# Performance work log

Measured on AMD Instinct MI355X. Metric: run time of the kernel, lower is better.

The kernel has to match this reference:

```python
import jax, jax.numpy as jnp
import numpy as np

SR = 44100.0
BS, NT, SEQ = 2, 16, 262144
REV_N, TAPS = 65536, 1023

EQ_R = [(-12., 12.), (20., 2000.), (0.1, 5.0),
        (-12., 12.), (80., 2000.), (0.1, 5.0),
        (-12., 12.), (2000., 8000.), (0.1, 5.0),
        (-12., 12.), (8000., 12000.), (0.1, 5.0),
        (-12., 12.), (12000., 21050.), (0.1, 5.0),
        (-12., 12.), (6000., 21050.), (0.1, 5.0)]
COMP_R = [(-60., 0.), (1., 10.), (5., 250.), (10., 250.), (3., 12.), (0., 6.)]
TRACK_R = np.array([(-48., 48.)] + EQ_R + COMP_R + [(-80., 12.), (0., 1.)], np.float32)
MASTER_R = np.array([(-48., 48.)] + EQ_R + COMP_R + [(-48., 48.)], np.float32)


def _pow2(n):
    return 1 << int(np.ceil(np.log2(n)))


def _denorm(p, r):
    lo = jnp.asarray(r[:, 0])
    hi = jnp.asarray(r[:, 1])
    return p * (hi - lo) + lo


def _biquad(g_db, fc, q, ftype):
    # RBJ cookbook biquads, coefficients normalized by a0
    A = 10.0 ** (g_db / 40.0)
    w0 = 2.0 * np.pi * (fc / SR)
    al = jnp.sin(w0) / (2.0 * q)
    c = jnp.cos(w0)
    sA = jnp.sqrt(A)
    if ftype == 'low_shelf':
        b0 = A * ((A + 1) - (A - 1) * c + 2 * sA * al)
        b1 = 2 * A * ((A - 1) - (A + 1) * c)
        b2 = A * ((A + 1) - (A - 1) * c - 2 * sA * al)
        a0 = (A + 1) + (A - 1) * c + 2 * sA * al
        a1 = -2 * ((A - 1) + (A + 1) * c)
        a2 = (A + 1) + (A - 1) * c - 2 * sA * al
    elif ftype == 'high_shelf':
        b0 = A * ((A + 1) + (A - 1) * c + 2 * sA * al)
        b1 = -2 * A * ((A - 1) + (A + 1) * c)
        b2 = A * ((A + 1) + (A - 1) * c - 2 * sA * al)
        a0 = (A + 1) - (A - 1) * c + 2 * sA * al
        a1 = 2 * ((A - 1) - (A + 1) * c)
        a2 = (A + 1) - (A - 1) * c - 2 * sA * al
    else:  # peaking
        b0 = 1 + al * A
        b1 = -2 * c
        b2 = 1 - al * A
        a0 = 1 + al / A
        a1 = -2 * c
        a2 = 1 - al / A
    b = jnp.stack([b0, b1, b2], -1) / a0[..., None]
    a = jnp.stack([a0, a1, a2], -1) / a0[..., None]
    return b, a


def _apply_eq(x, p):
    # 6-section cascaded biquad EQ applied via frequency sampling (as dasp_pytorch does).
    # x: (..., S); p: (..., 18) broadcastable with x's leading dims.
    S = x.shape[-1]
    nfft = _pow2(2 * S - 1)
    nf = nfft // 2 + 1
    w = jnp.arange(nf, dtype=jnp.float32) * (2.0 * np.pi / nfft)
    z1 = jnp.exp(-1j * w)
    z2 = z1 * z1
    H = jnp.ones((nf,), jnp.complex64)
    for k, ftype in enumerate(['low_shelf', 'peaking', 'peaking', 'peaking', 'peaking', 'high_shelf']):
        b, a = _biquad(p[..., 3 * k], p[..., 3 * k + 1], p[..., 3 * k + 2], ftype)
        num = b[..., 0:1] + b[..., 1:2] * z1 + b[..., 2:3] * z2
        den = a[..., 0:1] + a[..., 1:2] * z1 + a[..., 2:3] * z2
        H = H * (num / den)
    X = jnp.fft.rfft(x, nfft)
    return jnp.fft.irfft(X * H, nfft)[..., :S].astype(x.dtype)


def _apply_comp(x, p, lookahead):
    # soft-knee compressor; gain smoothed by one-pole (attack) via frequency sampling.
    S = x.shape[-1]
    nfft = _pow2(2 * S - 1)
    nf = nfft // 2 + 1
    th, ratio, at_ms, rel_ms, knee, makeup = [p[..., i:i + 1] for i in range(6)]
    x_db = 20.0 * jnp.log10(jnp.maximum(jnp.abs(x), 1e-8))
    d = x_db - th
    x_sc = jnp.where(2.0 * d < -knee, x_db,
                     jnp.where(2.0 * jnp.abs(d) <= knee,
                               x_db + (1.0 / ratio - 1.0) * (d + knee / 2.0) ** 2 / (2.0 * knee),
                               th + d / ratio))
    g_c = x_sc - x_db  # gain reduction in dB (<= 0)
    alpha = jnp.exp(-jnp.log(9.0) / (SR * at_ms * 1e-3))  # (..., 1)
    w = jnp.arange(nf, dtype=jnp.float32) * (2.0 * np.pi / nfft)
    H = (1.0 - alpha) / (1.0 - alpha * jnp.exp(-1j * w))
    g_s = jnp.fft.irfft(jnp.fft.rfft(g_c, nfft) * H, nfft)[..., :S]
    if lookahead > 0:
        tail = jnp.repeat(g_s[..., -1:], lookahead, axis=-1)
        g_s = jnp.concatenate([g_s[..., lookahead:], tail], axis=-1)
    return (x * 10.0 ** ((g_s + makeup) / 20.0)).astype(x.dtype)


def _reverb(x, noise, fb, gains, decays, mix):
    # noise-shaped reverberation: 12 octave-band filtered noise bursts with
    # exponential decays summed into an IR, FFT-convolved with x, wet/dry mix.
    S = x.shape[-1]
    nL = _pow2(REV_N + TAPS - 1)
    filt = jnp.fft.irfft(jnp.fft.rfft(noise, nL) * jnp.fft.rfft(fb, nL), nL)
    filt = filt[..., TAPS - 1:TAPS - 1 + REV_N]  # (bs, 2, 12, REV_N) 'valid' part
    t = jnp.linspace(0.0, 1.0, REV_N)
    dec = decays * 10.0 + 1.0  # (bs, 12)
    env = jnp.exp(-dec[:, None, :, None] * t)
    ir = (filt * env * gains[:, None, :, None]).mean(axis=2)  # (bs, 2, REV_N)
    n2 = _pow2(S + REV_N - 1)
    wet = jnp.fft.irfft(jnp.fft.rfft(x, n2) * jnp.fft.rfft(ir, n2), n2)[..., :S]
    m = mix[:, None, None]
    return (1.0 - m) * x + m * wet


def _firwin_lp(numtaps, fc, fs):
    n = np.arange(numtaps) - (numtaps - 1) / 2.0
    h = (2.0 * fc / fs) * np.sinc(2.0 * fc / fs * n)
    h = h * np.hamming(numtaps)
    return h / h.sum()


def _octave_fb():
    centers = [31.5, 63., 125., 250., 500., 1000., 2000., 4000., 8000., 16000.]
    nyq = SR / 2.0
    filts = [_firwin_lp(TAPS, 22.3, SR)]  # lowpass below lowest octave
    for fc in centers:
        f1 = fc / np.sqrt(2.0)
        f2 = min(fc * np.sqrt(2.0), 0.999 * nyq)
        filts.append(_firwin_lp(TAPS, f2, SR) - _firwin_lp(TAPS, f1, SR))
    hp = -_firwin_lp(TAPS, 18000.0, SR)
    hp[(TAPS - 1) // 2] += 1.0  # highpass = delta - lowpass
    filts.append(hp)
    return np.stack(filts).astype(np.float32)  # (12, TAPS)


def _forward(tracks, track_params, fx_bus_params, master_bus_params, reverb_noise, fb):
    tpd = _denorm(track_params, TRACK_R)    # (bs, NT, 27)
    mpd = _denorm(master_bus_params, MASTER_R)  # (bs, 26)
    fxp = fx_bus_params  # reverb ranges are (0,1): denorm is identity

    x = tracks * 10.0 ** (tpd[..., 0:1] / 20.0)          # input fader
    x = _apply_eq(x, tpd[..., 1:19])                      # 6-band parametric EQ
    x = _apply_comp(x, tpd[..., 19:25], 2048)             # compressor, lookahead 2048

    theta = tpd[..., 26] * (np.pi / 2)                    # constant-power panner
    gl = jnp.sqrt(((np.pi / 2) - theta) * (2.0 / np.pi) * jnp.cos(theta))
    gr = jnp.sqrt(theta * (2.0 / np.pi) * jnp.sin(theta))
    panned = jnp.stack([x * gl[..., None], x * gr[..., None]], axis=1)  # (bs, 2, NT, S)

    master = panned.sum(axis=2)                           # (bs, 2, S)
    send = 10.0 ** (tpd[..., 25] / 20.0)                  # fx bus sends
    fx_in = (panned * send[:, None, :, None]).sum(axis=2)
    master = master + _reverb(fx_in, reverb_noise, fb, fxp[:, :12], fxp[:, 12:24], fxp[:, 24])

    master = master * 10.0 ** (mpd[:, 0, None, None] / 20.0)   # master input fader
    master = _apply_eq(master, mpd[:, None, 1:19])
    master = _apply_comp(master, mpd[:, None, 19:25], 1024)
    master = master * 10.0 ** (mpd[:, 25, None, None] / 20.0)  # output fader
    return panned, master


def setup_inputs() -> dict:
    key = jax.random.key(0)
    k = jax.random.split(key, 5)
    tracks = 0.1 * jax.random.normal(k[0], (BS, NT, SEQ), jnp.float32)
    track_params = jax.random.uniform(k[1], (BS, NT, 27), jnp.float32)
    fx_bus_params = jax.random.uniform(k[2], (BS, 25), jnp.float32)
    master_bus_params = jax.random.uniform(k[3], (BS, 26), jnp.float32)
    reverb_noise = jax.random.normal(k[4], (BS, 2, 12, REV_N + TAPS - 1), jnp.float32)
    fb = jnp.asarray(_octave_fb())
    return {'tracks': tracks, 'track_params': track_params, 'fx_bus_params': fx_bus_params,
            'master_bus_params': master_bus_params, 'reverb_noise': reverb_noise, 'fb': fb}


def reference(tracks, track_params, fx_bus_params, master_bus_params, reverb_noise, fb):
    return _forward(tracks, track_params, fx_bus_params, master_bus_params, reverb_noise, fb)
```

## Files before the change

### kernel.cpp

```cpp
#include <hip/hip_runtime.h>

#define DEVFN __device__ __forceinline__

constexpr int SEQ = 262144;
constexpr int REV_N = 65536;
constexpr int TAPS = 1023;
constexpr int NOISE_LEN = REV_N + TAPS - 1;

constexpr int NS_T = 32, L_T = 128, C_T = 2048;
constexpr int NS_M = 4,  L_M = 64,  C_M = 4096;
constexpr int LA_T = 2048, LA_M = 1024;

constexpr int OUT_MASTER_OFF = 16777216;

constexpr int PADX = 65552;
constexpr int XBL  = 327744;
constexpr int IRPAD = 4096;
constexpr int IRL  = 73728;
constexpr int PADN = 2016;
constexpr int XNL  = 68640;
constexpr int FPAD = 2048;
constexpr int FBL  = 4160;

#define C_DB  0.16609640474436813f
#define C_LOG 6.0205999132796239f
#define PI_D  3.14159265358979323846

typedef __attribute__((ext_vector_type(8)))  short short8v;
typedef __attribute__((ext_vector_type(16))) float f32x16;

struct SigP {
  float g_in;
  float cb0[6], cb1[6], cb2[6], ca1[6], ca2[6];
  float alpha, oma;
  float th, invr, knee, makeup;
  float g_out;
  float gl, gr, send;
};

constexpr size_t OFF_X   = 0;
constexpr size_t OFF_Y   = 33554432;
constexpr size_t OFF_FX  = 67108864;
constexpr size_t OFF_M0  = 71303168;
constexpr size_t OFF_FILT = OFF_X;
constexpr size_t OFF_IR   = OFF_X + 12582912;
constexpr size_t OFF_XM   = OFF_X + 16777216;
constexpr size_t OFF_M1   = OFF_Y;
constexpr size_t OFF_WP   = OFF_Y + 4194304;
constexpr size_t OFF_XB   = OFF_WP + 16777216;
constexpr size_t OFF_IR2  = OFF_XB + (size_t)4*XBL*2;
constexpr size_t OFF_XBN  = 58720256;
constexpr size_t OFF_FBV  = 65536000;
constexpr size_t OFF_E12 = OFF_FX;
constexpr size_t OFF_I12 = OFF_FX + 3145728;
constexpr size_t OFF_E1  = OFF_FX + 6291456;
constexpr size_t OFF_I1  = OFF_FX + 6553600;
constexpr size_t OFF_GL  = 75497472;
constexpr size_t OFF_PT  = OFF_GL + 1024;
constexpr size_t OFF_PM  = OFF_PT + 32*sizeof(SigP);
constexpr size_t OFF_ALT = (OFF_PM + 4*sizeof(SigP) + 7) & ~(size_t)7;
constexpr size_t OFF_ALM = OFF_ALT + 32*8;
constexpr size_t OFF_AT  = (OFF_ALM + 4*8 + 15) & ~(size_t)15;
constexpr size_t OFF_AM  = OFF_AT + 18432;

DEVFN int pq(int i){ return i + ((i >> 5) << 2); }
DEVFN int pqb(int i){ return i + ((i >> 5) << 3); }

DEVFN unsigned short f2bf(float f){
  unsigned int u = __float_as_uint(f);
  unsigned int r = (u + 0x7fffu + ((u >> 16) & 1u)) >> 16;
  return (unsigned short)r;
}
DEVFN float bf2f(unsigned short h){ return __uint_as_float(((unsigned int)h) << 16); }

DEVFN double dn(float p, double lo, double hi){ return (double)p*(hi-lo)+lo; }

__device__ void mk_sig(const float* p, int L, bool is_master,
                       SigP* sp, float* Tf, double* aL)
{
  const double flo[6] = {20.,80.,2000.,8000.,12000.,6000.};
  const double fhi[6] = {2000.,2000.,8000.,12000.,21050.,21050.};
  double gdb = dn(p[0], -48., 48.);
  sp->g_in = (float)exp2(gdb * 0.16609640474436813);
  double db0[6],db1[6],db2[6],da1[6],da2[6];
  for (int k=0;k<6;k++){
    double g  = dn(p[1+3*k], -12., 12.);
    double fc = dn(p[2+3*k], flo[k], fhi[k]);
    double q  = dn(p[3+3*k], 0.1, 5.0);
    double A  = pow(10.0, g/40.0);
    double w0 = 2.0*PI_D*(fc/44100.0);
    double al = sin(w0)/(2.0*q), co = cos(w0), sA = sqrt(A);
    double b0,b1,b2,a0,a1,a2;
    if (k==0){
      b0 = A*((A+1.0) - (A-1.0)*co + 2.0*sA*al);
      b1 = 2.0*A*((A-1.0) - (A+1.0)*co);
      b2 = A*((A+1.0) - (A-1.0)*co - 2.0*sA*al);
      a0 = (A+1.0) + (A-1.0)*co + 2.0*sA*al;
      a1 = -2.0*((A-1.0) + (A+1.0)*co);
      a2 = (A+1.0) + (A-1.0)*co - 2.0*sA*al;
    } else if (k==5){
      b0 = A*((A+1.0) + (A-1.0)*co + 2.0*sA*al);
      b1 = -2.0*A*((A-1.0) + (A+1.0)*co);
      b2 = A*((A+1.0) + (A-1.0)*co - 2.0*sA*al);
      a0 = (A+1.0) - (A-1.0)*co + 2.0*sA*al;
      a1 = 2.0*((A-1.0) - (A+1.0)*co);
      a2 = (A+1.0) - (A-1.0)*co - 2.0*sA*al;
    } else {
      b0 = 1.0 + al*A; b1 = -2.0*co; b2 = 1.0 - al*A;
      a0 = 1.0 + al/A; a1 = -2.0*co; a2 = 1.0 - al/A;
    }
    double ia0 = 1.0/a0;
    db0[k]=b0*ia0; db1[k]=b1*ia0; db2[k]=b2*ia0; da1[k]=a1*ia0; da2[k]=a2*ia0;
    sp->cb0[k]=(float)db0[k]; sp->cb1[k]=(float)db1[k]; sp->cb2[k]=(float)db2[k];
    sp->ca1[k]=(float)da1[k]; sp->ca2[k]=(float)da2[k];
  }
  for (int i=0;i<12;i++){
    double st[12]; for (int r=0;r<12;r++) st[r]=0.0; st[i]=1.0;
    double ns[12];
    double yprev=0.0, pm1=0.0, pm2=0.0;
    for (int k=0;k<6;k++){
      double yk = db0[k]*yprev + db1[k]*pm1 + db2[k]*pm2 - da1[k]*st[2*k] - da2[k]*st[2*k+1];
      ns[2*k]=yk; ns[2*k+1]=st[2*k];
      pm1=st[2*k]; pm2=st[2*k+1];
      yprev=yk;
    }
    for (int r=0;r<12;r++) Tf[r*12+i]=(float)ns[r];
  }
  double th    = dn(p[19], -60., 0.);
  double ratio = dn(p[20], 1., 10.);
  double at    = dn(p[21], 5., 250.);
  double knee  = dn(p[23], 3., 12.);
  double mkup  = dn(p[24], 0., 6.);
  double alpha = exp(-log(9.0)/(44100.0*at*0.001));
  sp->alpha=(float)alpha; sp->oma=(float)(1.0-alpha);
  sp->th=(float)th; sp->invr=(float)(1.0/ratio); sp->knee=(float)knee; sp->makeup=(float)mkup;
  *aL = pow(alpha, (double)L);
  if (is_master){
    sp->g_out = (float)exp2(dn(p[25],-48.,48.)*0.16609640474436813);
    sp->gl=0.f; sp->gr=0.f; sp->send=0.f;
  } else {
    sp->g_out = 1.f;
    sp->send = (float)exp2(dn(p[25],-80.,12.)*0.16609640474436813);
    double th2 = dn(p[26],0.,1.)*(PI_D/2.0);
    sp->gl = (float)sqrt((PI_D/2.0-th2)*(2.0/PI_D)*cos(th2));
    sp->gr = (float)sqrt(th2*(2.0/PI_D)*sin(th2));
  }
}

__global__ __launch_bounds__(64) void k_params(const float* __restrict__ tp, const float* __restrict__ mp,
    SigP* Pt, SigP* Pm, float* AT, float* AM, double* aLt, double* aLm)
{
  int i = threadIdx.x;
  if (i < 32)       mk_sig(tp + i*27, L_T, false, &Pt[i], AT + i*144, &aLt[i]);
  else if (i < 36){ int j=i-32; mk_sig(mp + (j>>1)*26, L_M, true, &Pm[j], AM + j*144, &aLm[j]); }
}

__global__ __launch_bounds__(64) void k_power2(float* __restrict__ AT, float* __restrict__ AM)
{
  __shared__ float Ma[144], Mb[144];
  int b = blockIdx.x, t = threadIdx.x;
  float* A; int lg;
  if (b < 32){ A = AT + (size_t)b*144; lg = 7; }
  else       { A = AM + (size_t)(b-32)*144; lg = 6; }
  for (int idx=t; idx<144; idx+=64) Ma[idx]=A[idx];
  __syncthreads();
  int cur=0;
  for (int j=0;j<lg;j++){
    const float* src = cur? Mb:Ma;
    float* dst = cur? Ma:Mb;
    for (int idx=t; idx<144; idx+=64){
      int r=idx/12, cc=idx-r*12;
      float v=0.f;
      #pragma unroll
      for (int m=0;m<12;m++) v = fmaf(src[r*12+m], src[m*12+cc], v);
      dst[idx]=v;
    }
    __syncthreads();
    cur^=1;
  }
  const float* fin = cur? Mb:Ma;
  for (int idx=t; idx<144; idx+=64) A[idx]=fin[idx];
}

DEVFN float comp_gc(float y, float th, float invr, float kn){
  float av  = fmaxf(fabsf(y), 1e-8f);
  float xdb = C_LOG * __builtin_log2f(av);
  float d   = xdb - th;
  float w = (2.f*d < -kn) ? 0.f
          : ((2.f*fabsf(d) <= kn) ? (d+0.5f*kn)*(d+0.5f*kn)/(2.f*kn) : d);
  return (invr-1.f)*w;
}

__global__ __launch_bounds__(256) void k_eqA12(const float* __restrict__ in, const SigP* __restrict__ P,
    float* __restrict__ E12, int C, int L)
{
  int tid = blockIdx.x*256 + threadIdx.x;
  int sig = tid / C, c = tid - sig*C;
  const SigP* sp = P + sig;
  float B0[6],B1[6],B2[6],A1[6],A2[6];
  float g = sp->g_in;
  #pragma unroll
  for (int k=0;k<6;k++){
    float gg = (k==0)? g : 1.f;
    B0[k]=sp->cb0[k]*gg; B1[k]=sp->cb1[k]*gg; B2[k]=sp->cb2[k]*gg;
    A1[k]=sp->ca1[k];    A2[k]=sp->ca2[k];
  }
  const float* xp = in + (size_t)sig*SEQ + (size_t)c*L;
  float xm1=0.f, xm2=0.f;
  if (c){ xm1=xp[-1]; xm2=xp[-2]; }
  float s[12];
  #pragma unroll
  for (int r=0;r<12;r++) s[r]=0.f;
  for (int i=0;i<L;i+=4){
    float4 v = *(const float4*)(xp+i);
    #pragma unroll
    for (int u4=0;u4<4;u4++){
      float u = (u4==0)?v.x:(u4==1)?v.y:(u4==2)?v.z:v.w;
      float yprev=u, pm1=xm1, pm2=xm2;
      float ny[6];
      #pragma unroll
      for (int k=0;k<6;k++){
        float t0 = fmaf(B0[k],yprev, fmaf(B1[k],pm1, fmaf(B2[k],pm2, -A2[k]*s[2*k+1])));
        float yk = fmaf(-A1[k], s[2*k], t0);
        ny[k]=yk;
        pm1=s[2*k]; pm2=s[2*k+1];
        yprev=yk;
      }
      #pragma unroll
      for (int k=0;k<6;k++){ s[2*k+1]=s[2*k]; s[2*k]=ny[k]; }
      xm2=xm1; xm1=u;
    }
  }
  float* ep = E12 + (size_t)tid*12;
  #pragma unroll
  for (int r=0;r<12;r++) ep[r]=s[r];
}

__global__ __launch_bounds__(64) void k_scan12(const float* __restrict__ E, float* __restrict__ I,
    const float* __restrict__ Ab, int C, int Q, int lgQ)
{
  __shared__ float As[144], Pa[144], Pb[144];
  __shared__ float seg[64][12], ini[64][12];
  __shared__ float scur[12], stmp[12];
  int sig = blockIdx.x, t = threadIdx.x;
  const float* Asig = Ab + (size_t)sig*144;
  for (int idx=t; idx<144; idx+=64) As[idx]=Asig[idx];
  __syncthreads();
  const float* dp = E + ((size_t)sig*C + (size_t)t*Q)*12;
  float s[12];
  #pragma unroll
  for (int r=0;r<12;r++) s[r]=0.f;
  for (int j=0;j<Q;j++){
    const float* d = dp + j*12;
    float ns[12];
    #pragma unroll
    for (int r=0;r<12;r++){
      float v = d[r];
      #pragma unroll
      for (int cc=0;cc<12;cc++) v = fmaf(As[r*12+cc], s[cc], v);
      ns[r]=v;
    }
    #pragma unroll
    for (int r=0;r<12;r++) s[r]=ns[r];
  }
  #pragma unroll
  for (int r=0;r<12;r++) seg[t][r]=s[r];
  for (int idx=t; idx<144; idx+=64) Pa[idx]=As[idx];
  __syncthreads();
  int cur=0;
  for (int j=0;j<lgQ;j++){
    const float* src = cur? Pb:Pa;
    float* dst = cur? Pa:Pb;
    for (int idx=t; idx<144; idx+=64){
      int r=idx/12, cc=idx-r*12;
      float v=0.f;
      #pragma unroll
      for (int m=0;m<12;m++) v = fmaf(src[r*12+m], src[m*12+cc], v);
      dst[idx]=v;
    }
    __syncthreads();
    cur^=1;
  }
  const float* AQ = cur? Pb:Pa;
  if (t<12) scur[t]=0.f;
  __syncthreads();
  for (int u=0;u<64;u++){
    if (t<12){
      ini[u][t]=scur[t];
      float v = seg[u][t];
      #pragma unroll
      for (int cc=0;cc<12;cc++) v = fmaf(AQ[t*12+cc], scur[cc], v);
      stmp[t]=v;
    }
    __syncthreads();
    if (t<12) scur[t]=stmp[t];
    __syncthreads();
  }
  #pragma unroll
  for (int r=0;r<12;r++) s[r]=ini[t][r];
  float* op = I + ((size_t)sig*C + (size_t)t*Q)*12;
  for (int j=0;j<Q;j++){
    float* o = op + j*12;
    #pragma unroll
    for (int r=0;r<12;r++) o[r]=s[r];
    const float* d = dp + j*12;
    float ns[12];
    #pragma unroll
    for (int r=0;r<12;r++){
      float v = d[r];
      #pragma unroll
      for (int cc=0;cc<12;cc++) v = fmaf(As[r*12+cc], s[cc], v);
      ns[r]=v;
    }
    #pragma unroll
    for (int r=0;r<12;r++) s[r]=ns[r];
  }
}

__global__ __launch_bounds__(64) void k_scan1p(const float* __restrict__ endst, float* __restrict__ inits,
    const double* __restrict__ aL, int C, int Q, int lgQ)
{
  __shared__ double ag[64], ins[64];
  int sig = blockIdx.x; int t = threadIdx.x;
  double a = aL[sig];
  const float* dp = endst + (size_t)sig*C + (size_t)t*Q;
  double e=0.0;
  for (int j=0;j<Q;j++) e = a*e + (double)dp[j];
  ag[t]=e;
  __syncthreads();
  if (t == 0){
    double p=a;
    for (int j=0;j<lgQ;j++) p = p*p;
    double s=0.0;
    for (int u=0;u<64;u++){
      ins[u]=s;
      s = p*s + ag[u];
    }
  }
  __syncthreads();
  double s = ins[t];
  float* op = inits + (size_t)sig*C + (size_t)t*Q;
  for (int j=0;j<Q;j++){ op[j]=(float)s; s = a*s + (double)dp[j]; }
}

__global__ __launch_bounds__(256) void k_eqC12(const float* __restrict__ in, float* __restrict__ yout,
    const SigP* __restrict__ P, const float* __restrict__ I12, float* __restrict__ E1, int C, int L)
{
  int tid = blockIdx.x*256 + threadIdx.x;
  int sig = tid / C, c = tid - sig*C;
  const SigP* sp = P + sig;
  float B0[6],B1[6],B2[6],A1[6],A2[6];
  float g = sp->g_in;
  #pragma unroll
  for (int k=0;k<6;k++){
    float gg = (k==0)? g : 1.f;
    B0[k]=sp->cb0[k]*gg; B1[k]=sp->cb1[k]*gg; B2[k]=sp->cb2[k]*gg;
    A1[k]=sp->ca1[k];    A2[k]=sp->ca2[k];
  }
  float al=sp->alpha, oma=sp->oma, th=sp->th, invr=sp->invr, kn=sp->knee;
  size_t base = (size_t)sig*SEQ + (size_t)c*L;
  const float* xp = in + base;
  float* op = yout + base;
  float xm1=0.f, xm2=0.f;
  if (c){ xm1=xp[-1]; xm2=xp[-2]; }
  const float* ip = I12 + (size_t)tid*12;
  float s[12];
  #pragma unroll
  for (int r=0;r<12;r++) s[r]=ip[r];
  float gacc=0.f;
  for (int i=0;i<L;i+=4){
    float4 v = *(const float4*)(xp+i);
    float4 o;
    #pragma unroll
    for (int u4=0;u4<4;u4++){
      float u = (u4==0)?v.x:(u4==1)?v.y:(u4==2)?v.z:v.w;
      float yprev=u, pm1=xm1, pm2=xm2;
      float ny[6];
      #pragma unroll
      for (int k=0;k<6;k++){
        float t0 = fmaf(B0[k],yprev, fmaf(B1[k],pm1, fmaf(B2[k],pm2, -A2[k]*s[2*k+1])));
        float yk = fmaf(-A1[k], s[2*k], t0);
        ny[k]=yk;
        pm1=s[2*k]; pm2=s[2*k+1];
        yprev=yk;
      }
      #pragma unroll
      for (int k=0;k<6;k++){ s[2*k+1]=s[2*k]; s[2*k]=ny[k]; }
      xm2=xm1; xm1=u;
      float y5 = ny[5];
      if (u4==0) o.x=y5; else if (u4==1) o.y=y5; else if (u4==2) o.z=y5; else o.w=y5;
      gacc = fmaf(al, gacc, oma*comp_gc(y5,th,invr,kn));
    }
    *(float4*)(op+i) = o;
  }
  E1[tid]=gacc;
}

__global__ __launch_bounds__(256) void k_smoothcomp(const float* __restrict__ yin,
    const SigP* __restrict__ P, const float* __restrict__ inits1, float* __restrict__ gslast,
    float* __restrict__ outp, int C, int L, int lac)
{
  int tid = blockIdx.x*256 + threadIdx.x;
  int sig = tid / C, c = tid - sig*C;
  const SigP* sp = P + sig;
  float al=sp->alpha, oma=sp->oma, th=sp->th, invr=sp->invr, kn=sp->knee;
  float mk=sp->makeup, go=sp->g_out;
  size_t base = (size_t)sig*SEQ + (size_t)c*L;
  const float* xp = yin + base;
  bool wr = (c >= lac);
  size_t ob = wr ? (base - (size_t)lac*L) : 0;
  const float* yp = yin + ob;
  float* op = outp + ob;
  float gsv = inits1[tid];
  for (int i=0;i<L;i+=4){
    float4 v = *(const float4*)(xp+i);
    float4 gf;
    gsv = fmaf(al, gsv, oma*comp_gc(v.x,th,invr,kn)); gf.x=gsv;
    gsv = fmaf(al, gsv, oma*comp_gc(v.y,th,invr,kn)); gf.y=gsv;
    gsv = fmaf(al, gsv, oma*comp_gc(v.z,th,invr,kn)); gf.z=gsv;
    gsv = fmaf(al, gsv, oma*comp_gc(v.w,th,invr,kn)); gf.w=gsv;
    if (wr){
      float4 y2 = *(const float4*)(yp+i);
      float4 o;
      o.x = y2.x * __builtin_exp2f((gf.x+mk)*C_DB) * go;
      o.y = y2.y * __builtin_exp2f((gf.y+mk)*C_DB) * go;
      o.z = y2.z * __builtin_exp2f((gf.z+mk)*C_DB) * go;
      o.w = y2.w * __builtin_exp2f((gf.w+mk)*C_DB) * go;
      *(float4*)(op+i) = o;
    }
  }
  if (c == C-1) gslast[sig] = gsv;
}

__global__ __launch_bounds__(256) void k_comptail(const float* __restrict__ yin, const float* __restrict__ gslast,
    const SigP* __restrict__ P, float* __restrict__ outp, int la)
{
  int q = blockIdx.x*256 + threadIdx.x;
  int per = la/4;
  int sig = q / per;
  int r = (q - sig*per)*4;
  int n = SEQ - la + r;
  const SigP* sp = P + sig;
  float f = __builtin_exp2f((gslast[sig]+sp->makeup)*C_DB) * sp->g_out;
  size_t base = (size_t)sig*SEQ + n;
  float4 v = *(const float4*)(yin+base);
  float4 o = { v.x*f, v.y*f, v.z*f, v.w*f };
  *(float4*)(outp+base) = o;
}

__global__ __launch_bounds__(256) void k_pan(const float* __restrict__ y, const SigP* __restrict__ P,
    float* __restrict__ panned, float* __restrict__ m0, float* __restrict__ fx)
{
  int q = blockIdx.x*256 + threadIdx.x;
  int b = q / (SEQ/4);
  int n = (q - b*(SEQ/4))*4;
  float4 aL={0,0,0,0}, aR={0,0,0,0}, fL={0,0,0,0}, fR={0,0,0,0};
  for (int t=0;t<16;t++){
    const SigP* sp = P + b*16 + t;
    float gl=sp->gl, gr=sp->gr, sd=sp->send;
    float4 v = *(const float4*)(y + (size_t)(b*16+t)*SEQ + n);
    float4 pl = { v.x*gl, v.y*gl, v.z*gl, v.w*gl };
    float4 pr = { v.x*gr, v.y*gr, v.z*gr, v.w*gr };
    *(float4*)(panned + (size_t)(b*32+t)*SEQ + n)    = pl;
    *(float4*)(panned + (size_t)(b*32+16+t)*SEQ + n) = pr;
    aL.x+=pl.x; aL.y+=pl.y; aL.z+=pl.z; aL.w+=pl.w;
    aR.x+=pr.x; aR.y+=pr.y; aR.z+=pr.z; aR.w+=pr.w;
    fL.x=fmaf(pl.x,sd,fL.x); fL.y=fmaf(pl.y,sd,fL.y); fL.z=fmaf(pl.z,sd,fL.z); fL.w=fmaf(pl.w,sd,fL.w);
    fR.x=fmaf(pr.x,sd,fR.x); fR.y=fmaf(pr.y,sd,fR.y); fR.z=fmaf(pr.z,sd,fR.z); fR.w=fmaf(pr.w,sd,fR.w);
  }
  *(float4*)(m0 + (size_t)(b*2+0)*SEQ + n) = aL;
  *(float4*)(m0 + (size_t)(b*2+1)*SEQ + n) = aR;
  *(float4*)(fx + (size_t)(b*2+0)*SEQ + n) = fL;
  *(float4*)(fx + (size_t)(b*2+1)*SEQ + n) = fR;
}

__global__ __launch_bounds__(256) void k_ir2(const float* __restrict__ filt, const float* __restrict__ fxp,
    float* __restrict__ ir, unsigned short* __restrict__ IRV)
{
  int q = blockIdx.x*256 + threadIdx.x;
  int sig = q / (REV_N/4);
  int idx = q - sig*(REV_N/4);
  int i   = idx*4;
  int b = sig >> 1;
  float4 acc={0,0,0,0};
  const float ts = 1.0f/65535.0f;
  for (int band=0; band<12; band++){
    float gn  = fxp[b*25 + band];
    float dec = fxp[b*25 + 12 + band]*10.f + 1.f;
    float4 f = *(const float4*)(filt + ((size_t)(sig*12+band))*REV_N + i);
    float s = -dec*ts;
    float e0=expf(s*(float)i), e1=expf(s*(float)(i+1)), e2=expf(s*(float)(i+2)), e3=expf(s*(float)(i+3));
    acc.x = fmaf(gn*e0, f.x, acc.x);
    acc.y = fmaf(gn*e1, f.y, acc.y);
    acc.z = fmaf(gn*e2, f.z, acc.z);
    acc.w = fmaf(gn*e3, f.w, acc.w);
  }
  const float inv12 = 1.f/12.f;
  acc.x*=inv12; acc.y*=inv12; acc.z*=inv12; acc.w*=inv12;
  *(float4*)(ir + (size_t)sig*REV_N + i) = acc;
  unsigned short* iv = IRV + (size_t)sig*IRL;
  int base = IRPAD + REV_N-1 - i;
  iv[base]   = f2bf(acc.x);
  iv[base-1] = f2bf(acc.y);
  iv[base-2] = f2bf(acc.z);
  iv[base-3] = f2bf(acc.w);
  if (idx < 1024){
    *(ushort4*)(iv + idx*4) = make_ushort4(0,0,0,0);
  } else if (idx < 2048){
    *(ushort4*)(iv + IRPAD + REV_N + (idx-1024)*4) = make_ushort4(0,0,0,0);
  }
}

constexpr int P3_XB  = 4*XBL;
constexpr int P3_XBN = 48*XNL;
constexpr int P3_TOT = P3_XB + P3_XBN + 12*FBL;
__global__ __launch_bounds__(256) void k_prep3(const float* __restrict__ fx, const float* __restrict__ noise,
    const float* __restrict__ fb, unsigned short* __restrict__ XB, unsigned short* __restrict__ XBN,
    unsigned short* __restrict__ FBV)
{
  int q = blockIdx.x*256 + threadIdx.x;
  if (q < P3_XB){
    int sig = q / XBL;
    int m   = q - sig*XBL;
    int a = m - PADX;
    float v = (a >= 0 && a < SEQ) ? fx[(size_t)sig*SEQ + a] : 0.f;
    XB[(size_t)sig*XBL + m] = f2bf(v);
  } else if (q < P3_XB + P3_XBN){
    int q2 = q - P3_XB;
    int sig = q2 / XNL;
    int m   = q2 - sig*XNL;
    int a = m - PADN + 1022;
    float v = (a >= 0 && a < NOISE_LEN) ? noise[(size_t)sig*NOISE_LEN + a] : 0.f;
    XBN[(size_t)sig*XNL + m] = f2bf(v);
  } else if (q < P3_TOT){
    int q3 = q - P3_XB - P3_XBN;
    int band = q3 / FBL;
    int m = q3 - band*FBL;
    int a = m - FPAD;
    float v = (a >= 0 && a < TAPS) ? fb[band*TAPS + (TAPS-1 - a)] : 0.f;
    FBV[(size_t)band*FBL + m] = f2bf(v);
  }
}

__global__ __launch_bounds__(256,3) void k_firm(const unsigned short* __restrict__ XBN,
    const unsigned short* __restrict__ FBV, float* __restrict__ filt)
{
  __shared__ alignas(16) unsigned int xs0[4640];
  __shared__ alignas(16) unsigned int xs1[4640];
  __shared__ alignas(16) unsigned short sir[3840];
  int b = blockIdx.x;
  int ng  = b & 7;
  int sig = b >> 3;
  int band = sig % 12;
  int nblk = ng << 13;
  const int sbeg = -62;
  const int send = 126;

  int tid = threadIdx.x;
  int l  = tid & 63, wv = tid >> 6;
  int lj = l & 31, lg = l >> 5, ph = l & 1;
  int hl = (lj + 8*lg - ph) >> 1;
  int offB = 32*lj - 8*lg;
  const unsigned int* xbu = (const unsigned int*)(XBN + (size_t)sig*XNL);
  const unsigned short* irg = FBV + (size_t)band*FBL;
  const unsigned int* xsel = ph ? (const unsigned int*)xs1 : (const unsigned int*)xs0;

  f32x16 acc0 = {};
  f32x16 acc1 = {};
  int n0_0 = nblk + (wv*2+0)*1024;
  int n0_1 = nblk + (wv*2+1)*1024;

  for (int sa = sbeg; sa < send; sa += 128){
    int ns = send - sa; if (ns > 128) ns = 128;
    __syncthreads();
    int clo = nblk - 16*(sa + ns - 1);
    int ub  = (PADN + clo) >> 1;
    int nd  = ((nblk + 7168 + 46 - 16*sa) - clo)/2 + 2;
    for (int d = tid; d < nd; d += 256){
      unsigned int u0 = xbu[ub + d], u1 = xbu[ub + d + 1];
      xs0[d] = u0;
      xs1[d] = (u0 >> 16) | (u1 << 16);
    }
    int amin = 1022 - 16*(sa + ns - 1) - 992;
    int irlo = ((amin - 6) & ~7) + 6;
    int irspan = (1022 - 16*sa + 15) - irlo + 1;
    for (int r = tid; r < irspan; r += 256){
      sir[pqb(r)] = irg[FPAD + irlo + r];
    }
    __syncthreads();
    int db0 = ((n0_0 - clo) >> 1) - 8*sa + hl;
    int db1 = ((n0_1 - clo) >> 1) - 8*sa + hl;
    int Dh0 = 1022 - 16*sa - irlo;
    for (int ss = 0; ss < ns; ss++){
      int rB = (Dh0 - 16*ss) - offB;
      short8v bfrag = *(const short8v*)(sir + pqb(rB));
      union { unsigned int u[4]; short8v v; } a0, a1;
      int d0 = db0 - 8*ss, d1 = db1 - 8*ss;
      a0.u[0]=xsel[d0];   a0.u[1]=xsel[d0+1]; a0.u[2]=xsel[d0+2]; a0.u[3]=xsel[d0+3];
      a1.u[0]=xsel[d1];   a1.u[1]=xsel[d1+1]; a1.u[2]=xsel[d1+2]; a1.u[3]=xsel[d1+3];
      acc0 = __builtin_amdgcn_mfma_f32_32x32x16_bf16(a0.v, bfrag, acc0, 0, 0, 0);
      acc1 = __builtin_amdgcn_mfma_f32_32x32x16_bf16(a1.v, bfrag, acc1, 0, 0, 0);
    }
  }
  float* fp = filt + (size_t)sig*REV_N;
  #pragma unroll
  for (int reg = 0; reg < 16; reg++){
    int i = (reg & 3) + 8*(reg >> 2) + 4*lg;
    fp[n0_0 + i + 32*lj] = acc0[reg];
    fp[n0_1 + i + 32*lj] = acc1[reg];
  }
}

__global__ __launch_bounds__(256,2) void k_wetm(const unsigned short* __restrict__ XB,
    const unsigned short* __restrict__ IRV, unsigned short* __restrict__ WP)
{
  __shared__ alignas(16) unsigned int xs0[7200];
  __shared__ alignas(16) unsigned int xs1[7200];
  __shared__ alignas(16) unsigned short sir[7680];
  int b = blockIdx.x;
  int ng  = b & 15;
  int sig = (b >> 4) & 3;
  int kp  = b >> 6;
  int nblk = ng << 14;
  int sbeg = -254 + 544*kp;
  int send = sbeg + 544; if (send > 4097) send = 4097;

  int tid = threadIdx.x;
  int l  = tid & 63, wv = tid >> 6;
  int lj = l & 31, lg = l >> 5, ph = l & 1;
  int hl = (lj + 8*lg - ph) >> 1;
  int offB = 32*lj - 8*lg;
  const unsigned int* xbu = (const unsigned int*)(XB + (size_t)sig*XBL);
  const unsigned short* irg = IRV + (size_t)sig*IRL;
  const unsigned int* xsel = ph ? (const unsigned int*)xs1 : (const unsigned int*)xs0;

  f32x16 acc0 = {}, acc1 = {}, acc2 = {}, acc3 = {};
  int n0_w = nblk + wv*4096;

  for (int sa = sbeg; sa < send; sa += 128){
    int ns = send - sa; if (ns > 128) ns = 128;
    __syncthreads();
    int clo = nblk - 16*(sa + ns - 1);
    int ub  = (PADX + clo) >> 1;
    int nd  = (12336 + 16*(ns-1))/2 + 2;
    for (int d = tid; d < nd; d += 256){
      unsigned int u0 = xbu[ub + d], u1 = xbu[ub + d + 1];
      xs0[d] = u0;
      xs1[d] = (u0 >> 16) | (u1 << 16);
    }
    int amin = 65535 - 16*(sa + ns - 1) - 4064;
    int irlo = ((amin - 7) & ~7) + 7;
    int irspan = (65535 - 16*sa + 15) - irlo + 1;
    for (int r = tid; r < irspan; r += 256){
      sir[pqb(r)] = irg[IRPAD + irlo + r];
    }
    __syncthreads();
    int db0 = ((n0_w - clo) >> 1) - 8*sa + hl;
    int Dh0 = 65535 - 16*sa - irlo;
    for (int ss = 0; ss < ns; ss++){
      int rB = (Dh0 - 16*ss) - offB;
      int pb = pqb(rB);
      short8v bf0 = *(const short8v*)(sir + pb);
      short8v bf1 = *(const short8v*)(sir + pb - 1280);
      short8v bf2 = *(const short8v*)(sir + pb - 2560);
      short8v bf3 = *(const short8v*)(sir + pb - 3840);
      union { unsigned int u[4]; short8v v; } a0;
      int d0 = db0 - 8*ss;
      a0.u[0]=xsel[d0]; a0.u[1]=xsel[d0+1]; a0.u[2]=xsel[d0+2]; a0.u[3]=xsel[d0+3];
      acc0 = __builtin_amdgcn_mfma_f32_32x32x16_bf16(a0.v, bf0, acc0, 0, 0, 0);
      acc1 = __builtin_amdgcn_mfma_f32_32x32x16_bf16(a0.v, bf1, acc1, 0, 0, 0);
      acc2 = __builtin_amdgcn_mfma_f32_32x32x16_bf16(a0.v, bf2, acc2, 0, 0, 0);
      acc3 = __builtin_amdgcn_mfma_f32_32x32x16_bf16(a0.v, bf3, acc3, 0, 0, 0);
    }
  }
  unsigned short* wp = WP + ((size_t)(kp*4+sig))*SEQ;
  #pragma unroll
  for (int reg = 0; reg < 16; reg++){
    int i = (reg & 3) + 8*(reg >> 2) + 4*lg;
    int o = n0_w + i + 32*lj;
    wp[o]        = f2bf(acc0[reg]);
    wp[o + 1024] = f2bf(acc1[reg]);
    wp[o + 2048] = f2bf(acc2[reg]);
    wp[o + 3072] = f2bf(acc3[reg]);
  }
}

__global__ __launch_bounds__(256) void k_wetred(const unsigned short* __restrict__ wp, const float* __restrict__ fx,
    const float* __restrict__ m0, const float* __restrict__ fxp, float* __restrict__ m1)
{
  int q = blockIdx.x*256 + threadIdx.x;
  int sig = q / (SEQ/4);
  int n = (q - sig*(SEQ/4))*4;
  float mix = fxp[(sig>>1)*25+24];
  size_t ob = (size_t)sig*SEQ + n;
  float s0=0.f, s1=0.f, s2=0.f, s3=0.f;
  #pragma unroll
  for (int kp=0; kp<8; kp++){
    const unsigned short* p = wp + ((size_t)(kp*4+sig))*SEQ + n;
    s0 += bf2f(p[0]); s1 += bf2f(p[1]); s2 += bf2f(p[2]); s3 += bf2f(p[3]);
  }
  float4 w0 = *(const float4*)(m0+ob);
  float4 x0 = *(const float4*)(fx+ob);
  float om = 1.f - mix;
  float4 o;
  o.x = w0.x + om*x0.x + mix*s0;
  o.y = w0.y + om*x0.y + mix*s1;
  o.z = w0.z + om*x0.z + mix*s2;
  o.w = w0.w + om*x0.w + mix*s3;
  *(float4*)(m1+ob) = o;
}

extern "C" void kernel_launch(void* const* d_in, const int* in_sizes, int n_in,
                              void* d_out, int out_size, void* d_ws, size_t ws_size,
                              hipStream_t stream)
{
  const float* tracks = (const float*)d_in[0];
  const float* tp     = (const float*)d_in[1];
  const float* fxp    = (const float*)d_in[2];
  const float* mp     = (const float*)d_in[3];
  const float* noise  = (const float*)d_in[4];
  const float* fbp    = (const float*)d_in[5];
  float* out = (float*)d_out;
  char* w = (char*)d_ws;

  float*  X   = (float*)(w + OFF_X);
  float*  Y   = (float*)(w + OFF_Y);
  float*  FXb = (float*)(w + OFF_FX);
  float*  M0  = (float*)(w + OFF_M0);
  float*  E12 = (float*)(w + OFF_E12);
  float*  I12 = (float*)(w + OFF_I12);
  float*  E1  = (float*)(w + OFF_E1);
  float*  I1  = (float*)(w + OFF_I1);
  float*  GLt = (float*)(w + OFF_GL);
  float*  GLm = GLt + 32;
  SigP*   Pt  = (SigP*)(w + OFF_PT);
  SigP*   Pm  = (SigP*)(w + OFF_PM);
  double* aLt = (double*)(w + OFF_ALT);
  double* aLm = (double*)(w + OFF_ALM);
  float*  AT  = (float*)(w + OFF_AT);
  float*  AM  = (float*)(w + OFF_AM);
  float*  FILT= (float*)(w + OFF_FILT);
  float*  IR  = (float*)(w + OFF_IR);
  float*  XM  = (float*)(w + OFF_XM);
  float*  M1  = (float*)(w + OFF_M1);
  unsigned short* WPu = (unsigned short*)(w + OFF_WP);
  unsigned short* XB  = (unsigned short*)(w + OFF_XB);
  unsigned short* IRV = (unsigned short*)(w + OFF_IR2);
  unsigned short* XBN = (unsigned short*)(w + OFF_XBN);
  unsigned short* FBV = (unsigned short*)(w + OFF_FBV);

  k_params<<<1,64,0,stream>>>(tp, mp, Pt, Pm, AT, AM, aLt, aLm);
  k_power2<<<36,64,0,stream>>>(AT, AM);

  const int GT = NS_T*C_T/256;
  k_eqA12<<<GT,256,0,stream>>>(tracks, Pt, E12, C_T, L_T);
  k_scan12<<<NS_T,64,0,stream>>>(E12, I12, AT, C_T, C_T/64, 5);
  k_eqC12<<<GT,256,0,stream>>>(tracks, Y, Pt, I12, E1, C_T, L_T);
  k_scan1p<<<NS_T,64,0,stream>>>(E1, I1, aLt, C_T, C_T/64, 5);
  k_smoothcomp<<<GT,256,0,stream>>>(Y, Pt, I1, GLt, X, C_T, L_T, LA_T/L_T);
  k_comptail<<<NS_T*(LA_T/4)/256,256,0,stream>>>(Y, GLt, Pt, X, LA_T);
  k_pan<<<2*(SEQ/4)/256,256,0,stream>>>(X, Pt, out, M0, FXb);

  k_prep3<<<(P3_TOT+255)/256,256,0,stream>>>(FXb, noise, fbp, XB, XBN, FBV);
  k_firm<<<384,256,0,stream>>>(XBN, FBV, FILT);
  k_ir2<<<4*(REV_N/4)/256,256,0,stream>>>(FILT, fxp, IR, IRV);
  k_wetm<<<512,256,0,stream>>>(XB, IRV, WPu);
  k_wetred<<<4*(SEQ/4)/256,256,0,stream>>>(WPu, FXb, M0, fxp, M1);

  const int GM = NS_M*C_M/256;
  k_eqA12<<<GM,256,0,stream>>>(M1, Pm, E12, C_M, L_M);
  k_scan12<<<NS_M,64,0,stream>>>(E12, I12, AM, C_M, C_M/64, 6);
  k_eqC12<<<GM,256,0,stream>>>(M1, XM, Pm, I12, E1, C_M, L_M);
  k_scan1p<<<NS_M,64,0,stream>>>(E1, I1, aLm, C_M, C_M/64, 6);
  k_smoothcomp<<<GM,256,0,stream>>>(XM, Pm, I1, GLm, out + OUT_MASTER_OFF, C_M, L_M, LA_M/L_M);
  k_comptail<<<NS_M*(LA_M/4)/256,256,0,stream>>>(XM, GLm, Pm, out + OUT_MASTER_OFF, LA_M);
}
```

Measured before the change: 493.0 us.

## Restructure filterbank FIR MFMA kernel to reuse filter fragment across four output tiles

The filterbank FIR kernel swaps MFMA operand roles. The short filter becomes the A operand, held in two phase-shifted LDS copies. The whole input window for a 16K-sample output block is staged once into LDS, and each wave computes four 1024-sample tiles that share one filter fragment, which cuts LDS traffic and the multi-pass staging loop. Grid halves to 192 blocks, so fewer blocks may reduce occupancy and parallelism. Separately, the params and matrix-power kernels are merged into one launch to remove a kernel launch.

New measurement: 456.1 us. 1.08x faster.

```diff
diff --git a/kernel.cpp b/kernel.cpp
--- a/kernel.cpp
+++ b/kernel.cpp
@@ -147,22 +147,18 @@
   }
 }
 
-__global__ __launch_bounds__(64) void k_params(const float* __restrict__ tp, const float* __restrict__ mp,
+__global__ __launch_bounds__(64) void k_params2(const float* __restrict__ tp, const float* __restrict__ mp,
     SigP* Pt, SigP* Pm, float* AT, float* AM, double* aLt, double* aLm)
-{
-  int i = threadIdx.x;
-  if (i < 32)       mk_sig(tp + i*27, L_T, false, &Pt[i], AT + i*144, &aLt[i]);
-  else if (i < 36){ int j=i-32; mk_sig(mp + (j>>1)*26, L_M, true, &Pm[j], AM + j*144, &aLm[j]); }
-}
-
-__global__ __launch_bounds__(64) void k_power2(float* __restrict__ AT, float* __restrict__ AM)
 {
   __shared__ float Ma[144], Mb[144];
   int b = blockIdx.x, t = threadIdx.x;
-  float* A; int lg;
-  if (b < 32){ A = AT + (size_t)b*144; lg = 7; }
-  else       { A = AM + (size_t)(b-32)*144; lg = 6; }
-  for (int idx=t; idx<144; idx+=64) Ma[idx]=A[idx];
+  float* Aout; int lg;
+  if (t == 0){
+    if (b < 32) mk_sig(tp + b*27, L_T, false, &Pt[b], Ma, &aLt[b]);
+    else        mk_sig(mp + (b-32 >> 1)*26, L_M, true, &Pm[b-32], Ma, &aLm[b-32]);
+  }
+  if (b < 32){ Aout = AT + (size_t)b*144; lg = 7; }
+  else       { Aout = AM + (size_t)(b-32)*144; lg = 6; }
   __syncthreads();
   int cur=0;
   for (int j=0;j<lg;j++){
@@ -179,7 +175,7 @@
     cur^=1;
   }
   const float* fin = cur? Mb:Ma;
-  for (int idx=t; idx<144; idx+=64) A[idx]=fin[idx];
+  for (int idx=t; idx<144; idx+=64) Aout[idx]=fin[idx];
 }
 
 DEVFN float comp_gc(float y, float th, float invr, float kn){
@@ -542,72 +538,63 @@
   }
 }
 
-__global__ __launch_bounds__(256,3) void k_firm(const unsigned short* __restrict__ XBN,
+__global__ __launch_bounds__(256,3) void k_firm2(const unsigned short* __restrict__ XBN,
     const unsigned short* __restrict__ FBV, float* __restrict__ filt)
 {
-  __shared__ alignas(16) unsigned int xs0[4640];
-  __shared__ alignas(16) unsigned int xs1[4640];
-  __shared__ alignas(16) unsigned short sir[3840];
+  __shared__ alignas(16) unsigned short sx[21800];
+  __shared__ alignas(16) unsigned int rf0[560];
+  __shared__ alignas(16) unsigned int rf1[560];
   int b = blockIdx.x;
-  int ng  = b & 7;
-  int sig = b >> 3;
+  int ng  = b & 3;
+  int sig = b >> 2;
   int band = sig % 12;
-  int nblk = ng << 13;
-  const int sbeg = -62;
-  const int send = 126;
-
+  int nblk = ng << 14;
   int tid = threadIdx.x;
   int l  = tid & 63, wv = tid >> 6;
-  int lj = l & 31, lg = l >> 5, ph = l & 1;
-  int hl = (lj + 8*lg - ph) >> 1;
-  int offB = 32*lj - 8*lg;
-  const unsigned int* xbu = (const unsigned int*)(XBN + (size_t)sig*XNL);
-  const unsigned short* irg = FBV + (size_t)band*FBL;
-  const unsigned int* xsel = ph ? (const unsigned int*)xs1 : (const unsigned int*)xs0;
-
-  f32x16 acc0 = {};
-  f32x16 acc1 = {};
-  int n0_0 = nblk + (wv*2+0)*1024;
-  int n0_1 = nblk + (wv*2+1)*1024;
-
-  for (int sa = sbeg; sa < send; sa += 128){
-    int ns = send - sa; if (ns > 128) ns = 128;
-    __syncthreads();
-    int clo = nblk - 16*(sa + ns - 1);
-    int ub  = (PADN + clo) >> 1;
-    int nd  = ((nblk + 7168 + 46 - 16*sa) - clo)/2 + 2;
-    for (int d = tid; d < nd; d += 256){
-      unsigned int u0 = xbu[ub + d], u1 = xbu[ub + d + 1];
-      xs0[d] = u0;
-      xs1[d] = (u0 >> 16) | (u1 << 16);
-    }
-    int amin = 1022 - 16*(sa + ns - 1) - 992;
-    int irlo = ((amin - 6) & ~7) + 6;
-    int irspan = (1022 - 16*sa + 15) - irlo + 1;
-    for (int r = tid; r < irspan; r += 256){
-      sir[pqb(r)] = irg[FPAD + irlo + r];
-    }
-    __syncthreads();
-    int db0 = ((n0_0 - clo) >> 1) - 8*sa + hl;
-    int db1 = ((n0_1 - clo) >> 1) - 8*sa + hl;
-    int Dh0 = 1022 - 16*sa - irlo;
-    for (int ss = 0; ss < ns; ss++){
-      int rB = (Dh0 - 16*ss) - offB;
-      short8v bfrag = *(const short8v*)(sir + pqb(rB));
-      union { unsigned int u[4]; short8v v; } a0, a1;
-      int d0 = db0 - 8*ss, d1 = db1 - 8*ss;
-      a0.u[0]=xsel[d0];   a0.u[1]=xsel[d0+1]; a0.u[2]=xsel[d0+2]; a0.u[3]=xsel[d0+3];
-      a1.u[0]=xsel[d1];   a1.u[1]=xsel[d1+1]; a1.u[2]=xsel[d1+2]; a1.u[3]=xsel[d1+3];
-      acc0 = __builtin_amdgcn_mfma_f32_32x32x16_bf16(a0.v, bfrag, acc0, 0, 0, 0);
-      acc1 = __builtin_amdgcn_mfma_f32_32x32x16_bf16(a1.v, bfrag, acc1, 0, 0, 0);
-    }
-  }
-  float* fp = filt + (size_t)sig*REV_N;
+  int lj = l & 31, lg = l >> 5;
+  int ph = lj & 1;
+
+  const unsigned short* xg = XBN + (size_t)sig*XNL + (PADN + nblk - 1024);
+  for (int i = 4*tid; i < 17440; i += 1024){
+    ushort4 v = *(const ushort4*)(xg + i);
+    *(ushort4*)(sx + pqb(i)) = v;
+  }
+  const unsigned int* fbu = (const unsigned int*)(FBV + (size_t)band*FBL);
+  for (int d = tid; d < 560; d += 256){
+    unsigned int u0 = fbu[1004 + d], u1 = fbu[1004 + d + 1];
+    rf0[d] = u0;
+    rf1[d] = (u0 >> 16) | (u1 << 16);
+  }
+  __syncthreads();
+
+  const unsigned int* rsel = ph ? rf1 : rf0;
+  f32x16 acc0 = {}, acc1 = {}, acc2 = {}, acc3 = {};
+  int n0_w = wv*4096;
+
+  for (int ss = 0; ss < 67; ss++){
+    int d0 = (1094 - 16*ss - lj + 8*lg - ph) >> 1;
+    union { unsigned int u[4]; short8v v; } a0;
+    a0.u[0]=rsel[d0]; a0.u[1]=rsel[d0+1]; a0.u[2]=rsel[d0+2]; a0.u[3]=rsel[d0+3];
+    int e0 = n0_w + 1056 + 32*lj + 8*lg - 16*ss;
+    int pb = pqb(e0);
+    short8v bf0 = *(const short8v*)(sx + pb);
+    short8v bf1 = *(const short8v*)(sx + pb + 1280);
+    short8v bf2 = *(const short8v*)(sx + pb + 2560);
+    short8v bf3 = *(const short8v*)(sx + pb + 3840);
+    acc0 = __builtin_amdgcn_mfma_f32_32x32x16_bf16(a0.v, bf0, acc0, 0, 0, 0);
+    acc1 = __builtin_amdgcn_mfma_f32_32x32x16_bf16(a0.v, bf1, acc1, 0, 0, 0);
+    acc2 = __builtin_amdgcn_mfma_f32_32x32x16_bf16(a0.v, bf2, acc2, 0, 0, 0);
+    acc3 = __builtin_amdgcn_mfma_f32_32x32x16_bf16(a0.v, bf3, acc3, 0, 0, 0);
+  }
+  float* fp = filt + (size_t)sig*REV_N + nblk;
   #pragma unroll
   for (int reg = 0; reg < 16; reg++){
     int i = (reg & 3) + 8*(reg >> 2) + 4*lg;
-    fp[n0_0 + i + 32*lj] = acc0[reg];
-    fp[n0_1 + i + 32*lj] = acc1[reg];
+    int o = wv*4096 + i + 32*lj;
+    fp[o]        = acc0[reg];
+    fp[o + 1024] = acc1[reg];
+    fp[o + 2048] = acc2[reg];
+    fp[o + 3072] = acc3[reg];
   }
 }
 
@@ -749,8 +736,7 @@
   unsigned short* XBN = (unsigned short*)(w + OFF_XBN);
   unsigned short* FBV = (unsigned short*)(w + OFF_FBV);
 
-  k_params<<<1,64,0,stream>>>(tp, mp, Pt, Pm, AT, AM, aLt, aLm);
-  k_power2<<<36,64,0,stream>>>(AT, AM);
+  k_params2<<<36,64,0,stream>>>(tp, mp, Pt, Pm, AT, AM, aLt, aLm);
 
   const int GT = NS_T*C_T/256;
   k_eqA12<<<GT,256,0,stream>>>(tracks, Pt, E12, C_T, L_T);
@@ -762,7 +748,7 @@
   k_pan<<<2*(SEQ/4)/256,256,0,stream>>>(X, Pt, out, M0, FXb);
 
   k_prep3<<<(P3_TOT+255)/256,256,0,stream>>>(FXb, noise, fbp, XB, XBN, FBV);
-  k_firm<<<384,256,0,stream>>>(XBN, FBV, FILT);
+  k_firm2<<<192,256,0,stream>>>(XBN, FBV, FILT);
   k_ir2<<<4*(REV_N/4)/256,256,0,stream>>>(FILT, fxp, IR, IRV);
   k_wetm<<<512,256,0,stream>>>(XB, IRV, WPu);
   k_wetred<<<4*(SEQ/4)/256,256,0,stream>>>(WPu, FXb, M0, fxp, M1);
```
